# Kernel tuning notes

Hardware: AMD Instinct MI355X
Metric: run time of the kernel (lower is better)

The kernel has to match this reference:

```python
import jax, jax.numpy as jnp
import numpy as np

N = 100000      # nodes
E = 1250000     # edges
DIN = 128       # input_feature_dim
H = 64          # hidden_feature_dim
C = 16          # num_classes
BN_EPS = 1e-5


def _linear_init(key, fin, fout):
    # torch.nn.Linear default: U(-1/sqrt(fin), 1/sqrt(fin)); stored as [fin, fout] for x @ W
    s = 1.0 / np.sqrt(fin)
    kw, kb = jax.random.split(key)
    w = jax.random.uniform(kw, (fin, fout), jnp.float32, -s, s)
    b = jax.random.uniform(kb, (fout,), jnp.float32, -s, s)
    return w, b


def setup_inputs() -> dict:
    key = jax.random.key(0)
    ks = jax.random.split(key, 16)
    inp = {}
    inp["x"] = jax.random.normal(ks[0], (N, DIN), jnp.float32)
    src = jax.random.randint(ks[1], (E,), 0, N)
    dst = jax.random.randint(ks[2], (E,), 0, N)
    inp["edge_index"] = jnp.stack([src, dst]).astype(jnp.int64)
    inp["fc1_w"], inp["fc1_b"] = _linear_init(ks[3], DIN, H)
    dims = [(H, H), (H, H), (H, C)]
    for i, (fi, fo) in enumerate(dims):
        w, b = _linear_init(ks[4 + i], fi, fo)
        inp[f"conv{i}_w"] = w
        inp[f"conv{i}_b"] = b
        inp[f"bn{i}_g"] = jnp.ones((fo,), jnp.float32)
        inp[f"bn{i}_b"] = jnp.zeros((fo,), jnp.float32)
    inp["fc2_w"], inp["fc2_b"] = _linear_init(ks[7], C, C)
    return inp


def gcn_conv(h, w, b, src, dst, n):
    # PyG GCNConv: linear transform, add self-loops, symmetric normalization,
    # scatter-add messages from src into dst, then add bias.
    h = h @ w                                   # [N, out]
    loops = jnp.arange(n)
    s = jnp.concatenate([src, loops])           # [E+N]
    d = jnp.concatenate([dst, loops])
    deg = jax.ops.segment_sum(jnp.ones(s.shape[0], h.dtype), d, num_segments=n)
    dinv = jnp.where(deg > 0, jax.lax.rsqrt(deg), 0.0)
    norm = dinv[s] * dinv[d]                    # [E+N]
    msg = h[s] * norm[:, None]                  # [E+N, out] gather + scale
    out = jax.ops.segment_sum(msg, d, num_segments=n)
    return out + b


def batch_norm(x, gamma, beta):
    # BatchNorm1d in training mode: biased batch statistics over nodes
    mu = x.mean(axis=0)
    var = x.var(axis=0)
    return (x - mu) * jax.lax.rsqrt(var + BN_EPS) * gamma + beta


def reference(x, edge_index, fc1_w, fc1_b,
              conv0_w, conv0_b, bn0_g, bn0_b,
              conv1_w, conv1_b, bn1_g, bn1_b,
              conv2_w, conv2_b, bn2_g, bn2_b,
              fc2_w, fc2_b):
    src, dst = edge_index[0], edge_index[1]
    n = x.shape[0]
    h = jax.nn.relu(x @ fc1_w + fc1_b)
    layers = [(conv0_w, conv0_b, bn0_g, bn0_b),
              (conv1_w, conv1_b, bn1_g, bn1_b),
              (conv2_w, conv2_b, bn2_g, bn2_b)]
    for w, b, g, be in layers:
        h = jax.nn.relu(batch_norm(gcn_conv(h, w, b, src, dst, n), g, be))
    h = h @ fc2_w + fc2_b
    return jax.nn.log_softmax(h, axis=1)
```

## Files before the change

kernel.cpp:

```cpp
#include <hip/hip_runtime.h>

#define BN_EPS 1e-5f

typedef unsigned int uint32;

__device__ __forceinline__ void fma4(float4& a, float s, const float4& w) {
    a.x = fmaf(s, w.x, a.x); a.y = fmaf(s, w.y, a.y);
    a.z = fmaf(s, w.z, a.z); a.w = fmaf(s, w.w, a.w);
}

__device__ __forceinline__ float blo(uint32 p) { return __uint_as_float(p << 16); }
__device__ __forceinline__ float bhi(uint32 p) { return __uint_as_float(p & 0xFFFF0000u); }
__device__ __forceinline__ uint32 f2bf1(float f) {
    uint32 u = __float_as_uint(f);
    return (u + 0x7FFFu + ((u >> 16) & 1u)) >> 16;
}
__device__ __forceinline__ uint32 packbf(float a, float b) { return f2bf1(a) | (f2bf1(b) << 16); }


__global__ __launch_bounds__(256) void k_scan1(const int* __restrict__ deg, int* __restrict__ off,
                                               int* __restrict__ bsum, float* __restrict__ dinv, int n) {
    __shared__ int sh[256];
    int i = blockIdx.x * 256 + threadIdx.x;
    int v = (i < n) ? deg[i] : 0;
    if (i < n) dinv[i] = rsqrtf((float)v + 1.0f);
    sh[threadIdx.x] = v;
    __syncthreads();
    #pragma unroll
    for (int d = 1; d < 256; d <<= 1) {
        int t = (threadIdx.x >= d) ? sh[threadIdx.x - d] : 0;
        __syncthreads();
        sh[threadIdx.x] += t;
        __syncthreads();
    }
    if (i < n) off[i] = sh[threadIdx.x] - v;
    if (threadIdx.x == 255) bsum[blockIdx.x] = sh[255];
}

__global__ __launch_bounds__(512) void k_scan2(int* bsum, int nb) {
    __shared__ int sh[512];
    int v = (threadIdx.x < nb) ? bsum[threadIdx.x] : 0;
    sh[threadIdx.x] = v;
    __syncthreads();
    #pragma unroll
    for (int d = 1; d < 512; d <<= 1) {
        int t = (threadIdx.x >= d) ? sh[threadIdx.x - d] : 0;
        __syncthreads();
        sh[threadIdx.x] += t;
        __syncthreads();
    }
    if (threadIdx.x < nb) bsum[threadIdx.x] = sh[threadIdx.x] - v;
}

__global__ __launch_bounds__(256) void k_scan3(int* __restrict__ off, const int* __restrict__ bsum,
                                               int* __restrict__ cnt, int n, int e) {
    int i = blockIdx.x * 256 + threadIdx.x;
    if (i < n) { off[i] += bsum[blockIdx.x]; cnt[i] = 0; }
    if (i == 0) off[n] = e;
}


__global__ __launch_bounds__(256) void k_fc1_deg(const float* __restrict__ X, const float* __restrict__ W,
                                                 const float* __restrict__ bias, float* __restrict__ Y,
                                                 const int* __restrict__ dst, int* __restrict__ deg,
                                                 int n, int e, int nbLin) {
    constexpr int FIN = 128, FOUT = 64, KC = 64;
    constexpr int TX = FOUT / 4, TY = 256 / TX, RQ = 8, TILE_R = TY * RQ;
    __shared__ float Xs[TILE_R][KC + 4];
    __shared__ float Ws[KC][FOUT + 4];

    const int bid = blockIdx.x;
    const int twice = 2 * nbLin;
    bool isLin; int vid;
    if (bid < twice) { isLin = ((bid & 1) == 0); vid = bid >> 1; }
    else { isLin = false; vid = nbLin + (bid - twice); }

    if (!isLin) {
        const int ndeg = gridDim.x - nbLin;
        for (size_t i = (size_t)vid * 256 + threadIdx.x; i < (size_t)e; i += (size_t)ndeg * 256)
            atomicAdd(&deg[dst[i]], 1);
        return;
    }

    const int tx = threadIdx.x % TX;
    const int ty = threadIdx.x / TX;
    const float4 bb = *(const float4*)(bias + tx * 4);

    for (int r0 = vid * TILE_R; r0 < n; r0 += nbLin * TILE_R) {
        float4 acc[RQ];
        #pragma unroll
        for (int q = 0; q < RQ; ++q) acc[q] = bb;

        for (int kc = 0; kc < FIN; kc += KC) {
            __syncthreads();
            for (int idx = threadIdx.x; idx < TILE_R * (KC / 4); idx += 256) {
                int rr = idx / (KC / 4), k4 = idx % (KC / 4);
                int row = r0 + rr;
                float4 v = make_float4(0.f, 0.f, 0.f, 0.f);
                if (row < n) v = *(const float4*)(X + (size_t)row * FIN + kc + 4 * k4);
                *(float4*)(&Xs[rr][4 * k4]) = v;
            }
            for (int idx = threadIdx.x; idx < KC * (FOUT / 4); idx += 256) {
                int kk = idx / (FOUT / 4), c4 = idx % (FOUT / 4);
                *(float4*)(&Ws[kk][4 * c4]) = *(const float4*)(W + (size_t)(kc + kk) * FOUT + 4 * c4);
            }
            __syncthreads();

            #pragma unroll 4
            for (int k4 = 0; k4 < KC / 4; ++k4) {
                float4 w0 = *(const float4*)(&Ws[4*k4+0][tx*4]);
                float4 w1 = *(const float4*)(&Ws[4*k4+1][tx*4]);
                float4 w2 = *(const float4*)(&Ws[4*k4+2][tx*4]);
                float4 w3 = *(const float4*)(&Ws[4*k4+3][tx*4]);
                #pragma unroll
                for (int q = 0; q < RQ; ++q) {
                    float4 xv = *(const float4*)(&Xs[ty*RQ+q][4*k4]);
                    fma4(acc[q], xv.x, w0);
                    fma4(acc[q], xv.y, w1);
                    fma4(acc[q], xv.z, w2);
                    fma4(acc[q], xv.w, w3);
                }
            }
        }

        #pragma unroll
        for (int q = 0; q < RQ; ++q) {
            int row = r0 + ty * RQ + q;
            if (row < n) {
                float4 v = acc[q];
                v.x = fmaxf(v.x, 0.f); v.y = fmaxf(v.y, 0.f);
                v.z = fmaxf(v.z, 0.f); v.w = fmaxf(v.w, 0.f);
                *(float4*)(Y + (size_t)row * FOUT + tx * 4) = v;
            }
        }
    }
}


__global__ __launch_bounds__(256) void k_conv0_fill(const float* __restrict__ X, const float* __restrict__ W,
                                                    uint2* __restrict__ Yb, const float* __restrict__ dinv,
                                                    const int* __restrict__ src, const int* __restrict__ dst,
                                                    const int* __restrict__ off, int* __restrict__ cnt,
                                                    int* __restrict__ esrc, int n, int e, int nbLin) {
    constexpr int FIN = 64, FOUT = 64, KC = 64;
    constexpr int TX = FOUT / 4, TY = 256 / TX, RQ = 8, TILE_R = TY * RQ;
    __shared__ float Xs[TILE_R][KC + 4];
    __shared__ float Ws[KC][FOUT + 4];

    const int bid = blockIdx.x;
    const int twice = 2 * nbLin;
    bool isLin; int vid;
    if (bid < twice) { isLin = ((bid & 1) == 0); vid = bid >> 1; }
    else { isLin = false; vid = nbLin + (bid - twice); }

    if (!isLin) {
        const int nfl = gridDim.x - nbLin;
        for (size_t i = (size_t)vid * 256 + threadIdx.x; i < (size_t)e; i += (size_t)nfl * 256) {
            int d = dst[i];
            int slot = off[d] + atomicAdd(&cnt[d], 1);
            esrc[slot] = src[i];
        }
        return;
    }

    const int tx = threadIdx.x % TX;
    const int ty = threadIdx.x / TX;
    const int cq = tx >> 2, cr = tx & 3;

    for (int r0 = vid * TILE_R; r0 < n; r0 += nbLin * TILE_R) {
        float4 acc[RQ];
        #pragma unroll
        for (int q = 0; q < RQ; ++q) acc[q] = make_float4(0.f, 0.f, 0.f, 0.f);

        __syncthreads();
        for (int idx = threadIdx.x; idx < TILE_R * (KC / 4); idx += 256) {
            int rr = idx / (KC / 4), k4 = idx % (KC / 4);
            int row = r0 + rr;
            float4 v = make_float4(0.f, 0.f, 0.f, 0.f);
            if (row < n) v = *(const float4*)(X + (size_t)row * FIN + 4 * k4);
            *(float4*)(&Xs[rr][4 * k4]) = v;
        }
        for (int idx = threadIdx.x; idx < KC * (FOUT / 4); idx += 256) {
            int kk = idx / (FOUT / 4), c4 = idx % (FOUT / 4);
            *(float4*)(&Ws[kk][4 * c4]) = *(const float4*)(W + (size_t)kk * FOUT + 4 * c4);
        }
        __syncthreads();

        #pragma unroll 4
        for (int k4 = 0; k4 < KC / 4; ++k4) {
            float4 w0 = *(const float4*)(&Ws[4*k4+0][tx*4]);
            float4 w1 = *(const float4*)(&Ws[4*k4+1][tx*4]);
            float4 w2 = *(const float4*)(&Ws[4*k4+2][tx*4]);
            float4 w3 = *(const float4*)(&Ws[4*k4+3][tx*4]);
            #pragma unroll
            for (int q = 0; q < RQ; ++q) {
                float4 xv = *(const float4*)(&Xs[ty*RQ+q][4*k4]);
                fma4(acc[q], xv.x, w0);
                fma4(acc[q], xv.y, w1);
                fma4(acc[q], xv.z, w2);
                fma4(acc[q], xv.w, w3);
            }
        }

        #pragma unroll
        for (int q = 0; q < RQ; ++q) {
            int row = r0 + ty * RQ + q;
            if (row < n) {
                float4 v = acc[q];
                float dv = dinv[row];
                v.x *= dv; v.y *= dv; v.z *= dv; v.w *= dv;
                uint2 pk;
                pk.x = packbf(v.x, v.y);
                pk.y = packbf(v.z, v.w);
                Yb[(size_t)cq * n * 4 + (size_t)row * 4 + cr] = pk;
            }
        }
    }
}


template<int FIN, int FOUT, bool RELU, bool BIAS, bool BNIN, bool DSCALE, bool OBF>
__global__ __launch_bounds__(256) void k_linear(const float* __restrict__ X, const float* __restrict__ W,
                                                const float* __restrict__ bias, void* __restrict__ Yv,
                                                const float* __restrict__ S, const float* __restrict__ bng,
                                                const float* __restrict__ bnb, const float* __restrict__ dinv,
                                                float inv_n, int n) {
    constexpr int KC = 64;
    constexpr int TX = FOUT / 4;
    constexpr int TY = 256 / TX;
    constexpr int RQ = (FOUT == 64) ? 8 : 2;
    constexpr int TILE_R = TY * RQ;
    __shared__ float Xs[TILE_R][KC + 4];
    __shared__ float Ws[KC][FOUT + 4];
    __shared__ float scs[BNIN ? FIN : 4], sfs[BNIN ? FIN : 4];

    const int tx = threadIdx.x % TX;
    const int ty = threadIdx.x / TX;

    if (BNIN) {
        for (int c = threadIdx.x; c < FIN; c += 256) {
            float mu = S[c] * inv_n;
            float var = S[FIN + c] * inv_n - mu * mu;
            float is = rsqrtf(var + BN_EPS) * bng[c];
            scs[c] = is;
            sfs[c] = bnb[c] - mu * is;
        }
        __syncthreads();
    }

    float4 bb = make_float4(0.f, 0.f, 0.f, 0.f);
    if (BIAS) bb = *(const float4*)(bias + tx * 4);

    for (int r0 = blockIdx.x * TILE_R; r0 < n; r0 += gridDim.x * TILE_R) {
        float4 acc[RQ];
        #pragma unroll
        for (int q = 0; q < RQ; ++q) acc[q] = bb;

        for (int kc = 0; kc < FIN; kc += KC) {
            __syncthreads();
            for (int idx = threadIdx.x; idx < TILE_R * (KC / 4); idx += 256) {
                int rr = idx / (KC / 4), k4 = idx % (KC / 4);
                int row = r0 + rr;
                float4 v = make_float4(0.f, 0.f, 0.f, 0.f);
                if (row < n) v = *(const float4*)(X + (size_t)row * FIN + kc + 4 * k4);
                if (BNIN) {
                    int c = kc + 4 * k4;
                    v.x = fmaxf(fmaf(v.x, scs[c+0], sfs[c+0]), 0.f);
                    v.y = fmaxf(fmaf(v.y, scs[c+1], sfs[c+1]), 0.f);
                    v.z = fmaxf(fmaf(v.z, scs[c+2], sfs[c+2]), 0.f);
                    v.w = fmaxf(fmaf(v.w, scs[c+3], sfs[c+3]), 0.f);
                }
                *(float4*)(&Xs[rr][4 * k4]) = v;
            }
            for (int idx = threadIdx.x; idx < KC * (FOUT / 4); idx += 256) {
                int kk = idx / (FOUT / 4), c4 = idx % (FOUT / 4);
                *(float4*)(&Ws[kk][4 * c4]) = *(const float4*)(W + (size_t)(kc + kk) * FOUT + 4 * c4);
            }
            __syncthreads();

            #pragma unroll 4
            for (int k4 = 0; k4 < KC / 4; ++k4) {
                float4 w0 = *(const float4*)(&Ws[4*k4+0][tx*4]);
                float4 w1 = *(const float4*)(&Ws[4*k4+1][tx*4]);
                float4 w2 = *(const float4*)(&Ws[4*k4+2][tx*4]);
                float4 w3 = *(const float4*)(&Ws[4*k4+3][tx*4]);
                #pragma unroll
                for (int q = 0; q < RQ; ++q) {
                    float4 xv = *(const float4*)(&Xs[ty*RQ+q][4*k4]);
                    fma4(acc[q], xv.x, w0);
                    fma4(acc[q], xv.y, w1);
                    fma4(acc[q], xv.z, w2);
                    fma4(acc[q], xv.w, w3);
                }
            }
        }

        #pragma unroll
        for (int q = 0; q < RQ; ++q) {
            int row = r0 + ty * RQ + q;
            if (row < n) {
                float4 v = acc[q];
                if (RELU) {
                    v.x = fmaxf(v.x, 0.f); v.y = fmaxf(v.y, 0.f);
                    v.z = fmaxf(v.z, 0.f); v.w = fmaxf(v.w, 0.f);
                }
                if (DSCALE) {
                    float dv = dinv[row];
                    v.x *= dv; v.y *= dv; v.z *= dv; v.w *= dv;
                }
                if (OBF) {
                    uint2 pk;
                    pk.x = packbf(v.x, v.y);
                    pk.y = packbf(v.z, v.w);
                    if (FOUT == 64) {
                        int cq = tx >> 2, cr = tx & 3;
                        ((uint2*)Yv)[(size_t)cq * n * 4 + (size_t)row * 4 + cr] = pk;
                    } else {
                        ((uint2*)Yv)[(size_t)row * (FOUT / 4) + tx] = pk;
                    }
                } else {
                    *(float4*)((float*)Yv + (size_t)row * FOUT + tx * 4) = v;
                }
            }
        }
    }
}


__global__ __launch_bounds__(256) void k_accum64bf(const uint32* __restrict__ Tb, const int* __restrict__ esrc,
                                                   const int* __restrict__ off, const float* __restrict__ dinv,
                                                   const float* __restrict__ bias, float* __restrict__ Z,
                                                   float* __restrict__ S, int n, int e) {
    __shared__ uint32 ring[4][2][256];
    __shared__ float sA[4][16], sB[4][16];

    const int lane = threadIdx.x & 63;
    const int wid  = threadIdx.x >> 6;
    const int sb   = lane >> 3;
    const int cu   = lane & 7;
    const int ge   = lane >> 1;
    const int gh   = lane & 1;

    const int q   = blockIdx.x & 7;
    const int p   = q & 3;
    const int grp = q >> 2;
    const int bpq = gridDim.x >> 3;
    const int widx = (((blockIdx.x >> 3) + grp * bpq) << 2) + wid;
    const int NWc  = bpq * 8;

    const uint32* chunk  = Tb + (size_t)p * n * 8;
    const uint4*  chunk4 = (const uint4*)chunk;
    const float bc0 = bias[p * 16 + 2 * cu];
    const float bc1 = bias[p * 16 + 2 * cu + 1];
    float s1a = 0.f, s2a = 0.f, s1b = 0.f, s2b = 0.f;

    const int eS = (int)((long long)widx * e / NWc);
    const int eE = (int)((long long)(widx + 1) * e / NWc);

    int lo = 0, hi = n;
    while (lo < hi) { int mid = (lo + hi) >> 1; if (off[mid] < eS) lo = mid + 1; else hi = mid; }
    const int d0 = lo;
    int d1;
    if (widx == NWc - 1) d1 = n;
    else {
        lo = d0; hi = n;
        while (lo < hi) { int mid = (lo + hi) >> 1; if (off[mid] < eE) lo = mid + 1; else hi = mid; }
        d1 = lo;
    }

    if (d0 < d1) {
        const int e0 = off[d0];
        const int e1 = off[d1];
        const int nt = (e1 - e0 + 31) >> 5;
        uint32* slot0 = &ring[wid][0][0];
        uint32* slot1 = &ring[wid][1][0];

        int d = d0;
        int nxt = off[d + 1];
        uint32 selfw = chunk[(size_t)d * 8 + cu];
        float dv = dinv[d];
        float part0 = 0.f, part1 = 0.f;
        int ec = e0;

        auto tload = [&](int t) -> uint4 {
            int ei = min(e0 + t * 32 + ge, e1 - 1);
            int sn = __builtin_nontemporal_load(esrc + ei);
            return chunk4[(size_t)sn * 2 + gh];
        };

        uint4 B0, B1, B2;
        if (nt > 0) B0 = tload(0);
        if (nt > 1) B1 = tload(1);
        if (nt > 2) B2 = tload(2);

        for (int t = 0; t < nt; ++t) {
            uint32* sl = (t & 1) ? slot1 : slot0;
            uint4 cur = (t % 3 == 0) ? B0 : (t % 3 == 1) ? B1 : B2;
            *(uint4*)(sl + lane * 4) = cur;
            if (t + 3 < nt) {
                if (t % 3 == 0) B0 = tload(t + 3);
                else if (t % 3 == 1) B1 = tload(t + 3);
                else B2 = tload(t + 3);
            }
            const int te0 = e0 + t * 32;
            const int te1 = min(te0 + 32, e1);
            while (ec < te1) {
                int nend = min(nxt, te1);
                {
                    const uint32* pp = sl + (ec - te0 + sb) * 8 + cu;
                    for (int j = ec + sb; j < nend; j += 8, pp += 64) {
                        uint32 pw = *pp;
                        part0 += blo(pw);
                        part1 += bhi(pw);
                    }
                }
                ec = nend;
                if (ec == nxt) {
                    part0 += __shfl_xor(part0, 8);  part1 += __shfl_xor(part1, 8);
                    part0 += __shfl_xor(part0, 16); part1 += __shfl_xor(part1, 16);
                    part0 += __shfl_xor(part0, 32); part1 += __shfl_xor(part1, 32);
                    if (sb == 0) {
                        float z0 = fmaf(part0 + blo(selfw), dv, bc0);
                        float z1 = fmaf(part1 + bhi(selfw), dv, bc1);
                        __builtin_nontemporal_store(z0, Z + (size_t)d * 64 + p * 16 + 2 * cu);
                        __builtin_nontemporal_store(z1, Z + (size_t)d * 64 + p * 16 + 2 * cu + 1);
                        s1a += z0; s2a += z0 * z0; s1b += z1; s2b += z1 * z1;
                    }
                    ++d;
                    if (d < n) { nxt = off[d + 1]; selfw = chunk[(size_t)d * 8 + cu]; dv = dinv[d]; }
                    else nxt = e + 1;
                    part0 = 0.f; part1 = 0.f;
                }
            }
        }
        while (d < d1) {
            part0 += __shfl_xor(part0, 8);  part1 += __shfl_xor(part1, 8);
            part0 += __shfl_xor(part0, 16); part1 += __shfl_xor(part1, 16);
            part0 += __shfl_xor(part0, 32); part1 += __shfl_xor(part1, 32);
            if (sb == 0) {
                float z0 = fmaf(part0 + blo(selfw), dv, bc0);
                float z1 = fmaf(part1 + bhi(selfw), dv, bc1);
                __builtin_nontemporal_store(z0, Z + (size_t)d * 64 + p * 16 + 2 * cu);
                __builtin_nontemporal_store(z1, Z + (size_t)d * 64 + p * 16 + 2 * cu + 1);
                s1a += z0; s2a += z0 * z0; s1b += z1; s2b += z1 * z1;
            }
            ++d;
            if (d < d1) { selfw = chunk[(size_t)d * 8 + cu]; dv = dinv[d]; }
            part0 = 0.f; part1 = 0.f;
        }
    }

    if (sb == 0) {
        sA[wid][2 * cu] = s1a; sA[wid][2 * cu + 1] = s1b;
        sB[wid][2 * cu] = s2a; sB[wid][2 * cu + 1] = s2b;
    }
    __syncthreads();
    if (threadIdx.x < 16) {
        float t1 = 0.f, t2 = 0.f;
        #pragma unroll
        for (int w = 0; w < 4; ++w) { t1 += sA[w][threadIdx.x]; t2 += sB[w][threadIdx.x]; }
        atomicAdd(&S[p * 16 + threadIdx.x], t1);
        atomicAdd(&S[64 + p * 16 + threadIdx.x], t2);
    }
}


__global__ __launch_bounds__(256) void k_accum16bf(const uint2* __restrict__ Tb2, const int* __restrict__ esrc,
                                                   const int* __restrict__ off, const float* __restrict__ dinv,
                                                   const float* __restrict__ bias, float* __restrict__ Z,
                                                   float* __restrict__ S, int n) {
    const int lane = threadIdx.x & 63;
    const int wid  = threadIdx.x >> 6;
    const int lp   = lane & 3;
    const int es   = lane >> 2;
    const float4 bb = *(const float4*)(bias + 4 * lp);
    float st1[4] = {0.f,0.f,0.f,0.f}, st2[4] = {0.f,0.f,0.f,0.f};
    const uint2 z2 = make_uint2(0u, 0u);

    for (int dp = blockIdx.x * 4 + wid; 2 * dp < n; dp += gridDim.x * 4) {
        const int dA = 2 * dp, dB = 2 * dp + 1;
        const int oA0 = off[dA], oA1 = off[dA + 1];
        const int oB0 = oA1;
        const int oB1 = (dB < n) ? off[dB + 1] : oA1;

        float aA0=0.f, aA1=0.f, aA2=0.f, aA3=0.f;
        float aB0=0.f, aB1=0.f, aB2=0.f, aB3=0.f;
        int bA = oA0, bB = oB0;
        while (bA < oA1 || bB < oB1) {
            if (bA < oA1) {
                int i0 = bA + es;
                int s0 = (i0 < oA1) ? esrc[i0] : -1;
                uint2 p0 = (s0 >= 0) ? Tb2[(size_t)s0 * 4 + lp] : z2;
                aA0 += blo(p0.x); aA1 += bhi(p0.x); aA2 += blo(p0.y); aA3 += bhi(p0.y);
            }
            if (bB < oB1) {
                int i0 = bB + es;
                int s0 = (i0 < oB1) ? esrc[i0] : -1;
                uint2 p0 = (s0 >= 0) ? Tb2[(size_t)s0 * 4 + lp] : z2;
                aB0 += blo(p0.x); aB1 += bhi(p0.x); aB2 += blo(p0.y); aB3 += bhi(p0.y);
            }
            bA += 16; bB += 16;
        }

        #pragma unroll
        for (int sh = 4; sh <= 32; sh <<= 1) {
            aA0 += __shfl_xor(aA0, sh); aA1 += __shfl_xor(aA1, sh);
            aA2 += __shfl_xor(aA2, sh); aA3 += __shfl_xor(aA3, sh);
            aB0 += __shfl_xor(aB0, sh); aB1 += __shfl_xor(aB1, sh);
            aB2 += __shfl_xor(aB2, sh); aB3 += __shfl_xor(aB3, sh);
        }

        if (es == 0) {
            uint2 ps = Tb2[(size_t)dA * 4 + lp];
            float dv = dinv[dA];
            float4 zz;
            zz.x = fmaf(aA0 + blo(ps.x), dv, bb.x);
            zz.y = fmaf(aA1 + bhi(ps.x), dv, bb.y);
            zz.z = fmaf(aA2 + blo(ps.y), dv, bb.z);
            zz.w = fmaf(aA3 + bhi(ps.y), dv, bb.w);
            *(float4*)(Z + (size_t)dA * 16 + 4 * lp) = zz;
            st1[0] += zz.x; st2[0] += zz.x * zz.x;
            st1[1] += zz.y; st2[1] += zz.y * zz.y;
            st1[2] += zz.z; st2[2] += zz.z * zz.z;
            st1[3] += zz.w; st2[3] += zz.w * zz.w;
            if (dB < n) {
                uint2 pb = Tb2[(size_t)dB * 4 + lp];
                float dvB = dinv[dB];
                float4 zb;
                zb.x = fmaf(aB0 + blo(pb.x), dvB, bb.x);
                zb.y = fmaf(aB1 + bhi(pb.x), dvB, bb.y);
                zb.z = fmaf(aB2 + blo(pb.y), dvB, bb.z);
                zb.w = fmaf(aB3 + bhi(pb.y), dvB, bb.w);
                *(float4*)(Z + (size_t)dB * 16 + 4 * lp) = zb;
                st1[0] += zb.x; st2[0] += zb.x * zb.x;
                st1[1] += zb.y; st2[1] += zb.y * zb.y;
                st1[2] += zb.z; st2[2] += zb.z * zb.z;
                st1[3] += zb.w; st2[3] += zb.w * zb.w;
            }
        }
    }

    __shared__ float sh1[4][16], sh2[4][16];
    if (es == 0) {
        *(float4*)(&sh1[wid][4 * lp]) = make_float4(st1[0], st1[1], st1[2], st1[3]);
        *(float4*)(&sh2[wid][4 * lp]) = make_float4(st2[0], st2[1], st2[2], st2[3]);
    }
    __syncthreads();
    if (threadIdx.x < 16) {
        float t1 = 0.f, t2 = 0.f;
        #pragma unroll
        for (int w = 0; w < 4; ++w) { t1 += sh1[w][threadIdx.x]; t2 += sh2[w][threadIdx.x]; }
        atomicAdd(&S[threadIdx.x], t1);
        atomicAdd(&S[16 + threadIdx.x], t2);
    }
}


__global__ __launch_bounds__(256) void k_fc2_lsm(const float* __restrict__ Hin, const float* __restrict__ W,
                                                 const float* __restrict__ bias, const float* __restrict__ S,
                                                 const float* __restrict__ bng, const float* __restrict__ bnb,
                                                 float inv_n, float* __restrict__ out, int n) {
    __shared__ float Ws[256];
    __shared__ float bs[16], sc[16], sf[16];
    Ws[threadIdx.x] = W[threadIdx.x];
    if (threadIdx.x < 16) {
        int c = threadIdx.x;
        bs[c] = bias[c];
        float mu = S[c] * inv_n;
        float var = S[16 + c] * inv_n - mu * mu;
        float is = rsqrtf(var + BN_EPS) * bng[c];
        sc[c] = is;
        sf[c] = bnb[c] - mu * is;
    }
    __syncthreads();
    for (int row = blockIdx.x * 256 + threadIdx.x; row < n; row += gridDim.x * 256) {
        float h[16];
        const float4* hp = (const float4*)(Hin + (size_t)row * 16);
        #pragma unroll
        for (int q = 0; q < 4; ++q) {
            float4 h4 = hp[q];
            h[q*4+0] = h4.x; h[q*4+1] = h4.y; h[q*4+2] = h4.z; h[q*4+3] = h4.w;
        }
        #pragma unroll
        for (int k = 0; k < 16; ++k) h[k] = fmaxf(fmaf(h[k], sc[k], sf[k]), 0.0f);
        float o[16];
        #pragma unroll
        for (int c = 0; c < 16; ++c) {
            float acc = bs[c];
            #pragma unroll
            for (int k = 0; k < 16; ++k) acc += h[k] * Ws[k * 16 + c];
            o[c] = acc;
        }
        float m = o[0];
        #pragma unroll
        for (int c = 1; c < 16; ++c) m = fmaxf(m, o[c]);
        float ssum = 0.f;
        #pragma unroll
        for (int c = 0; c < 16; ++c) ssum += expf(o[c] - m);
        float lse = m + logf(ssum);
        float4* op = (float4*)(out + (size_t)row * 16);
        #pragma unroll
        for (int q = 0; q < 4; ++q) {
            float4 w4;
            w4.x = o[q*4+0] - lse; w4.y = o[q*4+1] - lse;
            w4.z = o[q*4+2] - lse; w4.w = o[q*4+3] - lse;
            op[q] = w4;
        }
    }
}


extern "C" void kernel_launch(void* const* d_in, const int* in_sizes, int n_in,
                              void* d_out, int out_size, void* d_ws, size_t ws_size,
                              hipStream_t stream) {
    const float* x      = (const float*)d_in[0];
    const int*   ei     = (const int*)d_in[1];
    const float* fc1_w  = (const float*)d_in[2];
    const float* fc1_b  = (const float*)d_in[3];
    const float* conv_w[3] = { (const float*)d_in[4],  (const float*)d_in[8],  (const float*)d_in[12] };
    const float* conv_b[3] = { (const float*)d_in[5],  (const float*)d_in[9],  (const float*)d_in[13] };
    const float* bn_g[3]   = { (const float*)d_in[6],  (const float*)d_in[10], (const float*)d_in[14] };
    const float* bn_b[3]   = { (const float*)d_in[7],  (const float*)d_in[11], (const float*)d_in[15] };
    const float* fc2_w  = (const float*)d_in[16];
    const float* fc2_b  = (const float*)d_in[17];

    const int n = in_sizes[0] / 128;
    const int e = in_sizes[1] / 2;
    const int* src = ei;
    const int* dst = ei + e;
    const float inv_n = 1.0f / (float)n;

    float*  A    = (float*)d_ws;
    float*  Bf   = A + (size_t)n * 64;
    uint32* Bb   = (uint32*)Bf;
    uint2*  Bb2  = (uint2*)Bf;
    float*  dinv = Bf + (size_t)n * 64;
    int*    deg  = (int*)(dinv + n);
    float*  stats = (float*)(deg + n);
    int*    off  = (int*)(stats + 384);
    int*    esrc = off + n + 1;
    int*    bsum = esrc + e;

    const int gN  = (n + 255) / 256;
    const int gAcc = 2048;
    const int gLin = (n + 127) / 128;
    const int nbLin = gLin;
    const int gFused = 2048;

    float* st[3] = { stats, stats + 128, stats + 256 };

    hipMemsetAsync(deg, 0, ((size_t)n + 384) * sizeof(int), stream);

    k_fc1_deg<<<gFused, 256, 0, stream>>>(x, fc1_w, fc1_b, A, dst, deg, n, e, nbLin);

    k_scan1<<<gN, 256, 0, stream>>>(deg, off, bsum, dinv, n);
    k_scan2<<<1, 512, 0, stream>>>(bsum, gN);
    k_scan3<<<gN, 256, 0, stream>>>(off, bsum, deg , n, e);

    k_conv0_fill<<<gFused, 256, 0, stream>>>(A, conv_w[0], Bb2, dinv, src, dst, off, deg , esrc, n, e, nbLin);
    k_accum64bf<<<gAcc, 256, 0, stream>>>(Bb, esrc, off, dinv, conv_b[0], A, st[0], n, e);

    k_linear<64, 64, false, false, true, true, true><<<gLin, 256, 0, stream>>>(
        A, conv_w[1], nullptr, Bb, st[0], bn_g[0], bn_b[0], dinv, inv_n, n);
    k_accum64bf<<<gAcc, 256, 0, stream>>>(Bb, esrc, off, dinv, conv_b[1], A, st[1], n, e);

    k_linear<64, 16, false, false, true, true, true><<<gLin, 256, 0, stream>>>(
        A, conv_w[2], nullptr, Bb2, st[1], bn_g[1], bn_b[1], dinv, inv_n, n);
    k_accum16bf<<<gAcc, 256, 0, stream>>>(Bb2, esrc, off, dinv, conv_b[2], A, st[2], n);

    k_fc2_lsm<<<gLin, 256, 0, stream>>>(A, fc2_w, fc2_b, st[2], bn_g[2], bn_b[2], inv_n, (float*)d_out, n);
}
```

Baseline: 409.4 us.

## Replace LDS ring-buffered edge pipeline with direct two-node interleaved gathers

Drops the per-wave LDS ring buffer and the three-stage register prefetch of edge tiles in the 64-wide bf16 aggregation kernel. Each wave now handles two destination nodes at a time, with eight edge slots per node loading source indices and bf16 words straight from global memory, interleaving the two nodes' loads to keep several in flight. This removes LDS traffic and tile bookkeeping, at the cost of fewer outstanding loads per wave and idle lanes when node degrees are uneven or small. A zeroing pass and an extra barrier are added before the stats reduction.

```diff
diff --git a/kernel.cpp b/kernel.cpp
--- a/kernel.cpp
+++ b/kernel.cpp
@@ -331,15 +331,12 @@
                                                    const int* __restrict__ off, const float* __restrict__ dinv,
                                                    const float* __restrict__ bias, float* __restrict__ Z,
                                                    float* __restrict__ S, int n, int e) {
-    __shared__ uint32 ring[4][2][256];
     __shared__ float sA[4][16], sB[4][16];
 
     const int lane = threadIdx.x & 63;
     const int wid  = threadIdx.x >> 6;
-    const int sb   = lane >> 3;
+    const int es   = lane >> 3;
     const int cu   = lane & 7;
-    const int ge   = lane >> 1;
-    const int gh   = lane & 1;
 
     const int q   = blockIdx.x & 7;
     const int p   = q & 3;
@@ -348,8 +345,7 @@
     const int widx = (((blockIdx.x >> 3) + grp * bpq) << 2) + wid;
     const int NWc  = bpq * 8;
 
-    const uint32* chunk  = Tb + (size_t)p * n * 8;
-    const uint4*  chunk4 = (const uint4*)chunk;
+    const uint32* chunk = Tb + (size_t)p * n * 8;
     const float bc0 = bias[p * 16 + 2 * cu];
     const float bc1 = bias[p * 16 + 2 * cu + 1];
     float s1a = 0.f, s2a = 0.f, s1b = 0.f, s2b = 0.f;
@@ -368,89 +364,59 @@
         d1 = lo;
     }
 
-    if (d0 < d1) {
-        const int e0 = off[d0];
-        const int e1 = off[d1];
-        const int nt = (e1 - e0 + 31) >> 5;
-        uint32* slot0 = &ring[wid][0][0];
-        uint32* slot1 = &ring[wid][1][0];
-
-        int d = d0;
-        int nxt = off[d + 1];
-        uint32 selfw = chunk[(size_t)d * 8 + cu];
-        float dv = dinv[d];
-        float part0 = 0.f, part1 = 0.f;
-        int ec = e0;
-
-        auto tload = [&](int t) -> uint4 {
-            int ei = min(e0 + t * 32 + ge, e1 - 1);
-            int sn = __builtin_nontemporal_load(esrc + ei);
-            return chunk4[(size_t)sn * 2 + gh];
-        };
-
-        uint4 B0, B1, B2;
-        if (nt > 0) B0 = tload(0);
-        if (nt > 1) B1 = tload(1);
-        if (nt > 2) B2 = tload(2);
-
-        for (int t = 0; t < nt; ++t) {
-            uint32* sl = (t & 1) ? slot1 : slot0;
-            uint4 cur = (t % 3 == 0) ? B0 : (t % 3 == 1) ? B1 : B2;
-            *(uint4*)(sl + lane * 4) = cur;
-            if (t + 3 < nt) {
-                if (t % 3 == 0) B0 = tload(t + 3);
-                else if (t % 3 == 1) B1 = tload(t + 3);
-                else B2 = tload(t + 3);
-            }
-            const int te0 = e0 + t * 32;
-            const int te1 = min(te0 + 32, e1);
-            while (ec < te1) {
-                int nend = min(nxt, te1);
-                {
-                    const uint32* pp = sl + (ec - te0 + sb) * 8 + cu;
-                    for (int j = ec + sb; j < nend; j += 8, pp += 64) {
-                        uint32 pw = *pp;
-                        part0 += blo(pw);
-                        part1 += bhi(pw);
-                    }
-                }
-                ec = nend;
-                if (ec == nxt) {
-                    part0 += __shfl_xor(part0, 8);  part1 += __shfl_xor(part1, 8);
-                    part0 += __shfl_xor(part0, 16); part1 += __shfl_xor(part1, 16);
-                    part0 += __shfl_xor(part0, 32); part1 += __shfl_xor(part1, 32);
-                    if (sb == 0) {
-                        float z0 = fmaf(part0 + blo(selfw), dv, bc0);
-                        float z1 = fmaf(part1 + bhi(selfw), dv, bc1);
-                        __builtin_nontemporal_store(z0, Z + (size_t)d * 64 + p * 16 + 2 * cu);
-                        __builtin_nontemporal_store(z1, Z + (size_t)d * 64 + p * 16 + 2 * cu + 1);
-                        s1a += z0; s2a += z0 * z0; s1b += z1; s2b += z1 * z1;
-                    }
-                    ++d;
-                    if (d < n) { nxt = off[d + 1]; selfw = chunk[(size_t)d * 8 + cu]; dv = dinv[d]; }
-                    else nxt = e + 1;
-                    part0 = 0.f; part1 = 0.f;
-                }
-            }
-        }
-        while (d < d1) {
-            part0 += __shfl_xor(part0, 8);  part1 += __shfl_xor(part1, 8);
-            part0 += __shfl_xor(part0, 16); part1 += __shfl_xor(part1, 16);
-            part0 += __shfl_xor(part0, 32); part1 += __shfl_xor(part1, 32);
-            if (sb == 0) {
-                float z0 = fmaf(part0 + blo(selfw), dv, bc0);
-                float z1 = fmaf(part1 + bhi(selfw), dv, bc1);
-                __builtin_nontemporal_store(z0, Z + (size_t)d * 64 + p * 16 + 2 * cu);
-                __builtin_nontemporal_store(z1, Z + (size_t)d * 64 + p * 16 + 2 * cu + 1);
-                s1a += z0; s2a += z0 * z0; s1b += z1; s2b += z1 * z1;
-            }
-            ++d;
-            if (d < d1) { selfw = chunk[(size_t)d * 8 + cu]; dv = dinv[d]; }
-            part0 = 0.f; part1 = 0.f;
-        }
-    }
-
-    if (sb == 0) {
+    for (int d = d0; d < d1; d += 2) {
+        const int dA = d, dB = d + 1;
+        const bool hasB = (dB < d1);
+        const int oA0 = off[dA], oA1 = off[dA + 1];
+        const int oB1 = hasB ? off[dB + 1] : oA1;
+
+        float a0 = 0.f, a1 = 0.f, b0 = 0.f, b1 = 0.f;
+        int iA = oA0 + es, iB = oA1 + es;
+        while (iA < oA1 || iB < oB1) {
+            if (iA < oA1) {
+                int s = __builtin_nontemporal_load(esrc + iA);
+                uint32 pw = chunk[(size_t)s * 8 + cu];
+                a0 += blo(pw); a1 += bhi(pw);
+            }
+            if (iB < oB1) {
+                int s = __builtin_nontemporal_load(esrc + iB);
+                uint32 pw = chunk[(size_t)s * 8 + cu];
+                b0 += blo(pw); b1 += bhi(pw);
+            }
+            iA += 8; iB += 8;
+        }
+
+        a0 += __shfl_xor(a0, 8);  a1 += __shfl_xor(a1, 8);
+        a0 += __shfl_xor(a0, 16); a1 += __shfl_xor(a1, 16);
+        a0 += __shfl_xor(a0, 32); a1 += __shfl_xor(a1, 32);
+        b0 += __shfl_xor(b0, 8);  b1 += __shfl_xor(b1, 8);
+        b0 += __shfl_xor(b0, 16); b1 += __shfl_xor(b1, 16);
+        b0 += __shfl_xor(b0, 32); b1 += __shfl_xor(b1, 32);
+
+        if (es == 0) {
+            uint32 sw = chunk[(size_t)dA * 8 + cu];
+            float dv = dinv[dA];
+            float z0 = fmaf(a0 + blo(sw), dv, bc0);
+            float z1 = fmaf(a1 + bhi(sw), dv, bc1);
+            __builtin_nontemporal_store(z0, Z + (size_t)dA * 64 + p * 16 + 2 * cu);
+            __builtin_nontemporal_store(z1, Z + (size_t)dA * 64 + p * 16 + 2 * cu + 1);
+            s1a += z0; s2a += z0 * z0; s1b += z1; s2b += z1 * z1;
+            if (hasB) {
+                uint32 swB = chunk[(size_t)dB * 8 + cu];
+                float dvB = dinv[dB];
+                float y0 = fmaf(b0 + blo(swB), dvB, bc0);
+                float y1 = fmaf(b1 + bhi(swB), dvB, bc1);
+                __builtin_nontemporal_store(y0, Z + (size_t)dB * 64 + p * 16 + 2 * cu);
+                __builtin_nontemporal_store(y1, Z + (size_t)dB * 64 + p * 16 + 2 * cu + 1);
+                s1a += y0; s2a += y0 * y0; s1b += y1; s2b += y1 * y1;
+            }
+        }
+    }
+
+    if (wid == 0 && lane < 16) { sA[0][lane]=0.f; sA[1][lane]=0.f; sA[2][lane]=0.f; sA[3][lane]=0.f;
+                                 sB[0][lane]=0.f; sB[1][lane]=0.f; sB[2][lane]=0.f; sB[3][lane]=0.f; }
+    __syncthreads();
+    if (es == 0) {
         sA[wid][2 * cu] = s1a; sA[wid][2 * cu + 1] = s1b;
         sB[wid][2 * cu] = s2a; sB[wid][2 * cu + 1] = s2b;
     }
```

New measurement: 513.3 us. +25.4%, slower.
